# Optimization experiments

Measured on AMD Instinct MI355X. Metric: run time of the kernel, lower is better.

Reference implementation:

```python
import jax, jax.numpy as jnp
import numpy as np

K = 3          # conv kernel size
PW = 4         # parallel window (pw_height == pw_width)
OC = 128       # out_channels
IC = 128       # in_channels
RANK = 256
STRIDE = PW - K + 1  # 2


def _sdk_weight_map(kernel):
    # kernel: [O, C, K, K] numpy. Concat all (top,left) zero-pad placements into PWxPW.
    O, C, k, _ = kernel.shape
    d = PW - k
    maps = []
    for top in range(d + 1):
        for left in range(d + 1):
            pk = np.zeros((O, C, PW, PW), dtype=kernel.dtype)
            pk[:, :, top:top + k, left:left + k] = kernel
            maps.append(pk.reshape(O, -1))
    return np.concatenate(maps, axis=0)  # [(d+1)^2 * O, C*PW*PW]


def setup_inputs() -> dict:
    rng = np.random.default_rng(0)
    kernel = (rng.standard_normal((OC, IC, K, K)) * 0.05).astype(np.float32)
    W = _sdk_weight_map(kernel)  # [512, 2048]
    u, s, vh = np.linalg.svd(W, full_matrices=False)
    Q = (u[:, :RANK] * s[:RANK]).astype(np.float32)   # u_t @ diag(s_t)
    R = vh[:RANK].astype(np.float32)
    key = jax.random.key(0)
    x = jax.random.normal(key, (32, 128, 64, 64), dtype=jnp.float32)
    return {"x": x, "Q": jnp.asarray(Q), "R": jnp.asarray(R)}


def _slice_and_forward(x, Q, R):
    N, C, H, Wd = x.shape
    s = STRIDE
    pad_v = (H + 2 - PW) % s
    pad_h = (Wd + 2 - PW) % s
    ov = -(-(H + 2 - PW) // s) + 1   # ceil div + 1 (matches math.ceil(...)+1)
    oh = -(-(Wd + 2 - PW) // s) + 1
    xp = jnp.pad(x, ((0, 0), (0, 0), (1, 1 + pad_v), (1, 1 + pad_h)))
    # im2col / unfold: feature layout C slowest, then (i, j) within window -> matches F.unfold
    wins = [xp[:, :, i:i + s * (ov - 1) + 1:s, j:j + s * (oh - 1) + 1:s]
            for i in range(PW) for j in range(PW)]
    patches = jnp.stack(wins, axis=2)                      # [N, C, PW*PW, ov, oh]
    flat = patches.reshape(N, C * PW * PW, ov * oh).transpose(0, 2, 1)  # [N, L, C*PW*PW]
    # F.linear(flat, Q @ R) == (flat @ R^T) @ Q^T  (apply low-rank factors sequentially)
    lin = jnp.einsum('nlr,mr->nlm', jnp.einsum('nlf,rf->nlr', flat, R), Q)  # [N, L, s*s*OC]
    lin = lin.reshape(N, ov, oh, s, s, OC).transpose(0, 1, 3, 2, 4, 5)
    lin = lin.reshape(N, H + pad_v // 2, Wd + pad_h // 2, OC)
    lin = lin.transpose(0, 3, 1, 2)                        # NHWC -> NCHW
    return lin[:, :, :H, :Wd]


def reference(x, Q, R):
    return _slice_and_forward(x, Q, R)
```

## Files before the change

### kernel.cpp

```cpp
#include <hip/hip_runtime.h>
#include <hip/hip_bf16.h>

typedef __attribute__((ext_vector_type(8))) short short8;
typedef __attribute__((ext_vector_type(4))) float f32x4;
typedef unsigned int uint;
typedef __attribute__((ext_vector_type(4))) uint uint4v;

#define AS1 __attribute__((address_space(1)))
#define AS3 __attribute__((address_space(3)))

#define QB_OFF  (1u << 20)
#define XPH_OFF (1310720u)

__device__ __forceinline__ uint bf16r(float f) {
    uint u = __float_as_uint(f);
    u += 0x7FFFu + ((u >> 16) & 1u);
    return u >> 16;
}
__device__ __forceinline__ uint pk2(float lo, float hi) {
    return bf16r(lo) | (bf16r(hi) << 16);
}

__global__ __launch_bounds__(256) void prep_kernel(
    const float* __restrict__ x, const float* __restrict__ Q, const float* __restrict__ R,
    char* __restrict__ Rp4, char* __restrict__ Qp4, char* __restrict__ xph)
{
    const int bid = blockIdx.x, tid = threadIdx.x;
    if (bid < 2048) {
        __shared__ float xt[128 * 65];
        const int n = bid >> 6, h = bid & 63;
        {
            const int c = tid >> 1, half = tid & 1;
            const float4* src = (const float4*)(x + (((size_t)(n * 128 + c) * 64 + h) * 64 + half * 32));
            #pragma unroll
            for (int q = 0; q < 8; ++q) {
                float4 v = src[q];
                float* d = &xt[c * 65 + half * 32 + q * 4];
                d[0] = v.x; d[1] = v.y; d[2] = v.z; d[3] = v.w;
            }
        }
        __syncthreads();
        {
            const int w = tid >> 2, cq = tid & 3;
            uint pw[16];
            #pragma unroll
            for (int m = 0; m < 16; ++m)
                pw[m] = pk2(xt[(cq * 32 + 2 * m) * 65 + w], xt[(cq * 32 + 2 * m + 1) * 65 + w]);
            char* dst = xph + (size_t)n * 1115136 + (size_t)(h + 1) * 16896 + (w + 1) * 256 + cq * 64;
            #pragma unroll
            for (int i = 0; i < 4; ++i) {
                uint4v q4 = { pw[4 * i], pw[4 * i + 1], pw[4 * i + 2], pw[4 * i + 3] };
                *(uint4v*)(dst + i * 16) = q4;
            }
        }
        if (tid < 32) {
            int side = tid >> 4, e = tid & 15;
            uint4v z = {0, 0, 0, 0};
            *(uint4v*)(xph + (size_t)n * 1115136 + (size_t)(h + 1) * 16896 + side * 65 * 256 + e * 16) = z;
        }
        if (h == 0) {
            uint4v z = {0, 0, 0, 0};
            #pragma unroll
            for (int it = 0; it < 9; ++it) {
                int idx = tid + it * 256;
                if (idx < 2112) {
                    int rr = (idx >= 1056) ? 65 : 0;
                    int jj = idx - (rr ? 1056 : 0);
                    int col = jj >> 4, e = jj & 15;
                    *(uint4v*)(xph + (size_t)n * 1115136 + (size_t)rr * 16896 + col * 256 + e * 16) = z;
                }
            }
        }
    } else if (bid < 2304) {
        int g = (bid - 2048) * 256 + tid;
        int s = g >> 10, rem = g & 1023;
        int cu = rem >> 8, col = rem & 255;
        const float* src = R + (size_t)col * 2048 + (((s & 3) * 32 + cu * 8) * 16 + (s >> 2));
        uint pw[4];
        #pragma unroll
        for (int m = 0; m < 4; ++m)
            pw[m] = pk2(src[(2 * m) * 16], src[(2 * m + 1) * 16]);
        uint4v q4 = { pw[0], pw[1], pw[2], pw[3] };
        *(uint4v*)(Rp4 + (size_t)g * 16) = q4;
    } else {
        int g = (bid - 2304) * 256 + tid;
        int ks = g >> 11, p = g & 2047;
        int col = p >> 2, cu = p & 3;
        const float4* s = (const float4*)(Q + (size_t)col * 256 + ks * 32 + cu * 8);
        float4 a = s[0], b = s[1];
        uint4v q4 = { pk2(a.x, a.y), pk2(a.z, a.w), pk2(b.x, b.y), pk2(b.z, b.w) };
        *(uint4v*)(Qp4 + (size_t)ks * 32768 + p * 16) = q4;
    }
}

__global__ __launch_bounds__(256, 2) void fused_kernel(
    const char* __restrict__ xph, const char* __restrict__ Rp4,
    const char* __restrict__ Qp4, float* __restrict__ out)
{
    extern __shared__ __align__(16) char lds[];

    const int blk = blockIdx.x;
    const int b = (blk & 7) * 64 + (blk >> 3);
    const int n = b >> 4, vt = b & 15;
    const int tid = threadIdx.x;
    const int wave = tid >> 6, lane = tid & 63;
    const int lr = lane & 15, kg = lane >> 4;
    const int lr7 = lr & 7;
    const int wn = wave;

    const char* xbase = xph + (size_t)n * 1115136;
    const int u16 = tid * 16;

    const int xrh = lane >> 5, xcl = lane & 31;
    const int xc0 = (4 * vt + 2 * xrh) * 16896 + (2 * xcl) * 256 + wave * 16;

    const int a0  = kg * 1024 + lr * 16;
    const int bb0 = kg * 4096 + wn * 1024 + lr * 16;

    const int t0 = (wn * 8 + (lr >> 3)) * 1024 + (lr & 7) * 2;

    int qoff[8];
    #pragma unroll
    for (int nf = 0; nf < 8; ++nf)
        qoff[nf] = ((wn >> 1) * 256 + (nf >> 2) * 128 + (wn & 1) * 64 + (nf & 3) * 16 + lr) * 64 + kg * 16;

#define BDMA(s_) { _Pragma("unroll") for (int q = 0; q < 4; ++q)                        \
        __builtin_amdgcn_global_load_lds(                                               \
            (const AS1 void*)(Rp4 + (size_t)(s_) * 16384 + q * 4096 + u16),             \
            (AS3 void*)(lds + 12288 + ((s_) % 3) * 16384 + q * 4096 + u16), 16, 0, 0); }
#define XDMA(s_) __builtin_amdgcn_global_load_lds(                                      \
        (const AS1 void*)(xbase + xc0 + ((s_) >> 4) * 16896 + (((s_) >> 2) & 3) * 256 + ((s_) & 3) * 64), \
        (AS3 void*)(lds + ((s_) % 3) * 4096 + u16), 16, 0, 0);

#define BAR(Nstr) { __builtin_amdgcn_sched_barrier(0);                                  \
        asm volatile("s_waitcnt vmcnt(" Nstr ") lgkmcnt(0)\n\ts_barrier" ::: "memory"); \
        __builtin_amdgcn_sched_barrier(0); }
#define LBAR { __builtin_amdgcn_sched_barrier(0);                                       \
        asm volatile("s_waitcnt lgkmcnt(0)\n\ts_barrier" ::: "memory");                 \
        __builtin_amdgcn_sched_barrier(0); }

    f32x4 acc[4][4];
    #pragma unroll
    for (int i = 0; i < 4; ++i)
        #pragma unroll
        for (int j = 0; j < 4; ++j) acc[i][j] = (f32x4)0.f;

    BDMA(0) XDMA(0) BDMA(1) XDMA(1)
    BAR("5")

    #pragma unroll
    for (int s = 0; s < 64; ++s) {
        if (s <= 61) { BDMA(s + 2) XDMA(s + 2) }
        const char* xs = lds + (s % 3) * 4096;
        const char* bs = lds + 12288 + (s % 3) * 16384;
        short8 af[4], bf[4];
        #pragma unroll
        for (int mf = 0; mf < 4; ++mf)
            af[mf] = *(const short8*)(xs + a0 + mf * 256);
        #pragma unroll
        for (int nf = 0; nf < 4; ++nf)
            bf[nf] = *(const short8*)(bs + bb0 + nf * 256);
        __builtin_amdgcn_s_setprio(1);
        #pragma unroll
        for (int nf = 0; nf < 4; ++nf)
            #pragma unroll
            for (int mf = 0; mf < 4; ++mf)
                acc[mf][nf] = __builtin_amdgcn_mfma_f32_16x16x32_bf16(af[mf], bf[nf], acc[mf][nf], 0, 0, 0);
        __builtin_amdgcn_s_setprio(0);
        if (s <= 61) { BAR("5") } else { BAR("0") }
    }

    #pragma unroll
    for (int mf = 0; mf < 4; ++mf)
        #pragma unroll
        for (int nf = 0; nf < 4; ++nf)
            #pragma unroll
            for (int r = 0; r < 4; ++r) {
                *(ushort*)(lds + t0 + nf * 2048 + (mf * 16 + kg * 4 + r) * 16) =
                    (ushort)bf16r(acc[mf][nf][r]);
            }
    LBAR

    f32x4 acc2[4][8];
    #pragma unroll
    for (int i = 0; i < 4; ++i)
        #pragma unroll
        for (int j = 0; j < 8; ++j) acc2[i][j] = (f32x4)0.f;
    #pragma unroll
    for (int ks = 0; ks < 8; ++ks) {
        short8 af2[4];
        #pragma unroll
        for (int mf = 0; mf < 4; ++mf)
            af2[mf] = *(const short8*)(lds + ks * 4096 + a0 + mf * 256);
        #pragma unroll
        for (int nf = 0; nf < 8; ++nf) {
            const short8 bq = *(const short8*)(Qp4 + (size_t)ks * 32768 + qoff[nf]);
            #pragma unroll
            for (int mf = 0; mf < 4; ++mf)
                acc2[mf][nf] = __builtin_amdgcn_mfma_f32_16x16x32_bf16(af2[mf], bq, acc2[mf][nf], 0, 0, 0);
        }
    }

    const int si = wn >> 1, ochalf = wn & 1;
    #pragma unroll
    for (int p = 0; p < 2; ++p) {
        LBAR
        #pragma unroll
        for (int mfh = 0; mfh < 2; ++mfh) {
            const int mf = 2 * p + mfh;
            #pragma unroll
            for (int q = 0; q < 4; ++q) {
                const int oc = ochalf * 64 + q * 16 + lr;
                const int ub = si * 32768 + oc * 256 + (((4 * mfh + kg) ^ lr7) << 5);
                f32x4 v0 = { acc2[mf][q][0], acc2[mf][4 + q][0], acc2[mf][q][1], acc2[mf][4 + q][1] };
                f32x4 v1 = { acc2[mf][q][2], acc2[mf][4 + q][2], acc2[mf][q][3], acc2[mf][4 + q][3] };
                *(f32x4*)(lds + ub) = v0;
                *(f32x4*)(lds + ub + 16) = v1;
            }
        }
        LBAR
        #pragma unroll
        for (int it = 0; it < 16; ++it) {
            int uidx = it * 256 + tid;
            int w4 = uidx & 15, oc = (uidx >> 4) & 127, sie = uidx >> 11;
            f32x4 v = *(const f32x4*)(lds + sie * 32768 + oc * 256 + ((w4 ^ (2 * (oc & 7))) << 4));
            *(f32x4*)(out + (size_t)n * 524288 + (size_t)oc * 4096
                          + (vt * 4 + p * 2 + sie) * 64 + w4 * 4) = v;
        }
    }
}

extern "C" void kernel_launch(void* const* d_in, const int* in_sizes, int n_in,
                              void* d_out, int out_size, void* d_ws, size_t ws_size,
                              hipStream_t stream) {
    const float* x = (const float*)d_in[0];
    const float* Q = (const float*)d_in[1];
    const float* R = (const float*)d_in[2];
    float* out = (float*)d_out;

    char* ws = (char*)d_ws;
    char* Rp4 = ws;
    char* Qp4 = ws + QB_OFF;
    char* xph = ws + XPH_OFF;

    prep_kernel<<<2368, 256, 0, stream>>>(x, Q, R, Rp4, Qp4, xph);
    fused_kernel<<<512, 256, 65536, stream>>>(xph, Rp4, Qp4, out);
}
```

Before: 89.42 us.

## Load GEMM1 fragments directly from global with register double-buffering, drop LDS staging

The first low-rank GEMM no longer stages x patches and R tiles through a triple-buffered LDS pipeline with per-step barriers. Each wave now loads its MFMA fragments straight from global memory into two register sets that alternate, so loads overlap compute without barriers. The second GEMM is split into two halves to lower live accumulator registers, its results are written directly to global instead of going through an LDS transpose, LDS drops to 32KB and the occupancy hint rises to 3 blocks. The risks are redundant global/L2 traffic, since waves no longer share staged tiles, and less coalesced output stores.

```diff
diff --git a/kernel.cpp b/kernel.cpp
--- a/kernel.cpp
+++ b/kernel.cpp
@@ -93,7 +93,7 @@
     }
 }
 
-__global__ __launch_bounds__(256, 2) void fused_kernel(
+__global__ __launch_bounds__(256, 3) void fused_kernel(
     const char* __restrict__ xph, const char* __restrict__ Rp4,
     const char* __restrict__ Qp4, float* __restrict__ out)
 {
@@ -105,128 +105,100 @@
     const int tid = threadIdx.x;
     const int wave = tid >> 6, lane = tid & 63;
     const int lr = lane & 15, kg = lane >> 4;
-    const int lr7 = lr & 7;
     const int wn = wave;
 
-    const char* xbase = xph + (size_t)n * 1115136;
-    const int u16 = tid * 16;
-
-    const int xrh = lane >> 5, xcl = lane & 31;
-    const int xc0 = (4 * vt + 2 * xrh) * 16896 + (2 * xcl) * 256 + wave * 16;
-
-    const int a0  = kg * 1024 + lr * 16;
-    const int bb0 = kg * 4096 + wn * 1024 + lr * 16;
-
-    const int t0 = (wn * 8 + (lr >> 3)) * 1024 + (lr & 7) * 2;
-
+    const char* xbase = xph + (size_t)n * 1115136 + (size_t)(4 * vt) * 16896;
+    const int xv0 = lr * 512 + kg * 16;
+    const int bv0 = kg * 4096 + (wn * 64 + lr) * 16;
+
+    f32x4 acc[4][4];
+    #pragma unroll
+    for (int i = 0; i < 4; ++i)
+        #pragma unroll
+        for (int j = 0; j < 4; ++j) acc[i][j] = (f32x4)0.f;
+
+    short8 afA[4], bfA[4], afB[4], bfB[4];
+
+#define LOADA(dst_, s_) { \
+        const char* xp_ = xbase + ((s_) >> 4) * 16896 + (((s_) >> 2) & 3) * 256 + ((s_) & 3) * 64 + xv0; \
+        dst_[0] = *(const short8*)(xp_);             \
+        dst_[1] = *(const short8*)(xp_ + 8192);      \
+        dst_[2] = *(const short8*)(xp_ + 33792);     \
+        dst_[3] = *(const short8*)(xp_ + 41984); }
+#define LOADB(dst_, s_) { \
+        const char* rp_ = Rp4 + (size_t)(s_) * 16384 + bv0; \
+        _Pragma("unroll") for (int nf = 0; nf < 4; ++nf) \
+            dst_[nf] = *(const short8*)(rp_ + nf * 256); }
+#define MFMA16(af_, bf_) { \
+        __builtin_amdgcn_s_setprio(1); \
+        _Pragma("unroll") for (int nf = 0; nf < 4; ++nf) \
+            _Pragma("unroll") for (int mf = 0; mf < 4; ++mf) \
+                acc[mf][nf] = __builtin_amdgcn_mfma_f32_16x16x32_bf16(af_[mf], bf_[nf], acc[mf][nf], 0, 0, 0); \
+        __builtin_amdgcn_s_setprio(0); }
+
+    LOADA(afA, 0) LOADB(bfA, 0)
+    LOADA(afB, 1) LOADB(bfB, 1)
+
+    #pragma unroll 4
+    for (int s = 0; s < 64; s += 2) {
+        MFMA16(afA, bfA);
+        if (s < 62) { LOADA(afA, s + 2) LOADB(bfA, s + 2) }
+        MFMA16(afB, bfB);
+        if (s <= 60) { LOADA(afB, s + 3) LOADB(bfB, s + 3) }
+    }
+
+    {
+        const int t0 = (wn * 8 + (lr >> 3)) * 1024 + (lr & 7) * 2;
+        #pragma unroll
+        for (int mf = 0; mf < 4; ++mf)
+            #pragma unroll
+            for (int nf = 0; nf < 4; ++nf)
+                #pragma unroll
+                for (int r = 0; r < 4; ++r)
+                    *(ushort*)(lds + t0 + nf * 2048 + (mf * 16 + kg * 4 + r) * 16) =
+                        (ushort)bf16r(acc[mf][nf][r]);
+    }
+    __syncthreads();
+
+    const int a2base = kg * 1024 + lr * 16;
     int qoff[8];
     #pragma unroll
     for (int nf = 0; nf < 8; ++nf)
         qoff[nf] = ((wn >> 1) * 256 + (nf >> 2) * 128 + (wn & 1) * 64 + (nf & 3) * 16 + lr) * 64 + kg * 16;
-
-#define BDMA(s_) { _Pragma("unroll") for (int q = 0; q < 4; ++q)                        \
-        __builtin_amdgcn_global_load_lds(                                               \
-            (const AS1 void*)(Rp4 + (size_t)(s_) * 16384 + q * 4096 + u16),             \
-            (AS3 void*)(lds + 12288 + ((s_) % 3) * 16384 + q * 4096 + u16), 16, 0, 0); }
-#define XDMA(s_) __builtin_amdgcn_global_load_lds(                                      \
-        (const AS1 void*)(xbase + xc0 + ((s_) >> 4) * 16896 + (((s_) >> 2) & 3) * 256 + ((s_) & 3) * 64), \
-        (AS3 void*)(lds + ((s_) % 3) * 4096 + u16), 16, 0, 0);
-
-#define BAR(Nstr) { __builtin_amdgcn_sched_barrier(0);                                  \
-        asm volatile("s_waitcnt vmcnt(" Nstr ") lgkmcnt(0)\n\ts_barrier" ::: "memory"); \
-        __builtin_amdgcn_sched_barrier(0); }
-#define LBAR { __builtin_amdgcn_sched_barrier(0);                                       \
-        asm volatile("s_waitcnt lgkmcnt(0)\n\ts_barrier" ::: "memory");                 \
-        __builtin_amdgcn_sched_barrier(0); }
-
-    f32x4 acc[4][4];
+    const int si = wn >> 1, ochalf = wn & 1;
+
     #pragma unroll
-    for (int i = 0; i < 4; ++i)
-        #pragma unroll
-        for (int j = 0; j < 4; ++j) acc[i][j] = (f32x4)0.f;
-
-    BDMA(0) XDMA(0) BDMA(1) XDMA(1)
-    BAR("5")
-
-    #pragma unroll
-    for (int s = 0; s < 64; ++s) {
-        if (s <= 61) { BDMA(s + 2) XDMA(s + 2) }
-        const char* xs = lds + (s % 3) * 4096;
-        const char* bs = lds + 12288 + (s % 3) * 16384;
-        short8 af[4], bf[4];
-        #pragma unroll
-        for (int mf = 0; mf < 4; ++mf)
-            af[mf] = *(const short8*)(xs + a0 + mf * 256);
-        #pragma unroll
-        for (int nf = 0; nf < 4; ++nf)
-            bf[nf] = *(const short8*)(bs + bb0 + nf * 256);
-        __builtin_amdgcn_s_setprio(1);
-        #pragma unroll
-        for (int nf = 0; nf < 4; ++nf)
-            #pragma unroll
-            for (int mf = 0; mf < 4; ++mf)
-                acc[mf][nf] = __builtin_amdgcn_mfma_f32_16x16x32_bf16(af[mf], bf[nf], acc[mf][nf], 0, 0, 0);
-        __builtin_amdgcn_s_setprio(0);
-        if (s <= 61) { BAR("5") } else { BAR("0") }
-    }
-
-    #pragma unroll
-    for (int mf = 0; mf < 4; ++mf)
-        #pragma unroll
-        for (int nf = 0; nf < 4; ++nf)
-            #pragma unroll
-            for (int r = 0; r < 4; ++r) {
-                *(ushort*)(lds + t0 + nf * 2048 + (mf * 16 + kg * 4 + r) * 16) =
-                    (ushort)bf16r(acc[mf][nf][r]);
-            }
-    LBAR
-
-    f32x4 acc2[4][8];
-    #pragma unroll
-    for (int i = 0; i < 4; ++i)
-        #pragma unroll
-        for (int j = 0; j < 8; ++j) acc2[i][j] = (f32x4)0.f;
-    #pragma unroll
-    for (int ks = 0; ks < 8; ++ks) {
-        short8 af2[4];
-        #pragma unroll
-        for (int mf = 0; mf < 4; ++mf)
-            af2[mf] = *(const short8*)(lds + ks * 4096 + a0 + mf * 256);
-        #pragma unroll
-        for (int nf = 0; nf < 8; ++nf) {
-            const short8 bq = *(const short8*)(Qp4 + (size_t)ks * 32768 + qoff[nf]);
-            #pragma unroll
-            for (int mf = 0; mf < 4; ++mf)
-                acc2[mf][nf] = __builtin_amdgcn_mfma_f32_16x16x32_bf16(af2[mf], bq, acc2[mf][nf], 0, 0, 0);
-        }
-    }
-
-    const int si = wn >> 1, ochalf = wn & 1;
-    #pragma unroll
-    for (int p = 0; p < 2; ++p) {
-        LBAR
-        #pragma unroll
-        for (int mfh = 0; mfh < 2; ++mfh) {
-            const int mf = 2 * p + mfh;
+    for (int mh2 = 0; mh2 < 2; ++mh2) {
+        f32x4 a2[2][8];
+        #pragma unroll
+        for (int u = 0; u < 2; ++u)
+            #pragma unroll
+            for (int j = 0; j < 8; ++j) a2[u][j] = (f32x4)0.f;
+        #pragma unroll
+        for (int ks = 0; ks < 8; ++ks) {
+            short8 af2[2];
+            af2[0] = *(const short8*)(lds + ks * 4096 + a2base + (mh2 * 2) * 256);
+            af2[1] = *(const short8*)(lds + ks * 4096 + a2base + (mh2 * 2 + 1) * 256);
+            #pragma unroll
+            for (int nf = 0; nf < 8; ++nf) {
+                const short8 bq = *(const short8*)(Qp4 + (size_t)ks * 32768 + qoff[nf]);
+                a2[0][nf] = __builtin_amdgcn_mfma_f32_16x16x32_bf16(af2[0], bq, a2[0][nf], 0, 0, 0);
+                a2[1][nf] = __builtin_amdgcn_mfma_f32_16x16x32_bf16(af2[1], bq, a2[1][nf], 0, 0, 0);
+            }
+        }
+        const int r_out = vt * 4 + mh2 * 2 + si;
+        float* ob = out + (size_t)n * 524288 + (size_t)r_out * 64;
+        #pragma unroll
+        for (int u = 0; u < 2; ++u)
             #pragma unroll
             for (int q = 0; q < 4; ++q) {
                 const int oc = ochalf * 64 + q * 16 + lr;
-                const int ub = si * 32768 + oc * 256 + (((4 * mfh + kg) ^ lr7) << 5);
-                f32x4 v0 = { acc2[mf][q][0], acc2[mf][4 + q][0], acc2[mf][q][1], acc2[mf][4 + q][1] };
-                f32x4 v1 = { acc2[mf][q][2], acc2[mf][4 + q][2], acc2[mf][q][3], acc2[mf][4 + q][3] };
-                *(f32x4*)(lds + ub) = v0;
-                *(f32x4*)(lds + ub + 16) = v1;
-            }
-        }
-        LBAR
-        #pragma unroll
-        for (int it = 0; it < 16; ++it) {
-            int uidx = it * 256 + tid;
-            int w4 = uidx & 15, oc = (uidx >> 4) & 127, sie = uidx >> 11;
-            f32x4 v = *(const f32x4*)(lds + sie * 32768 + oc * 256 + ((w4 ^ (2 * (oc & 7))) << 4));
-            *(f32x4*)(out + (size_t)n * 524288 + (size_t)oc * 4096
-                          + (vt * 4 + p * 2 + sie) * 64 + w4 * 4) = v;
-        }
+                float* o2 = ob + (size_t)oc * 4096 + u * 32 + kg * 8;
+                f32x4 v0 = { a2[u][q][0], a2[u][4 + q][0], a2[u][q][1], a2[u][4 + q][1] };
+                f32x4 v1 = { a2[u][q][2], a2[u][4 + q][2], a2[u][q][3], a2[u][4 + q][3] };
+                *(f32x4*)(o2) = v0;
+                *(f32x4*)(o2 + 4) = v1;
+            }
     }
 }
 
@@ -244,5 +216,5 @@
     char* xph = ws + XPH_OFF;
 
     prep_kernel<<<2368, 256, 0, stream>>>(x, Q, R, Rp4, Qp4, xph);
-    fused_kernel<<<512, 256, 65536, stream>>>(xph, Rp4, Qp4, out);
-}
+    fused_kernel<<<512, 256, 32768, stream>>>(xph, Rp4, Qp4, out);
+}
```

Result: slower. 130.1 us (+45.5%).

## Double block tile to 512 threads with 4-stage pipeline and direct output stores

Applied to the files above, without the earlier changes.

Each workgroup now processes twice as many output rows (128-row M tile split across 2x4 waves), so every R tile loaded into LDS is reused by twice as many rows. Grid size is halved and the block size doubled. The LDS ring grows from 3 to 4 stages with prefetch distance 3, and a barrier is added after the fragment loads. The epilogue drops the LDS transpose staging and writes accumulators straight to global memory, saving barriers and LDS traffic at the cost of less coalesced stores. LDS use rises to 96KB per block, which may limit occupancy.

```diff
diff --git a/kernel.cpp b/kernel.cpp
--- a/kernel.cpp
+++ b/kernel.cpp
@@ -93,51 +93,43 @@
     }
 }
 
-__global__ __launch_bounds__(256, 2) void fused_kernel(
+__global__ __launch_bounds__(512, 2) void fused_kernel(
     const char* __restrict__ xph, const char* __restrict__ Rp4,
     const char* __restrict__ Qp4, float* __restrict__ out)
 {
     extern __shared__ __align__(16) char lds[];
 
     const int blk = blockIdx.x;
-    const int b = (blk & 7) * 64 + (blk >> 3);
-    const int n = b >> 4, vt = b & 15;
+    const int b = (blk & 7) * 32 + (blk >> 3);
+    const int n = b >> 3, vt = b & 7;
     const int tid = threadIdx.x;
     const int wave = tid >> 6, lane = tid & 63;
     const int lr = lane & 15, kg = lane >> 4;
-    const int lr7 = lr & 7;
-    const int wn = wave;
+    const int wm = wave >> 2, wn = wave & 3;
 
     const char* xbase = xph + (size_t)n * 1115136;
     const int u16 = tid * 16;
 
-    const int xrh = lane >> 5, xcl = lane & 31;
-    const int xc0 = (4 * vt + 2 * xrh) * 16896 + (2 * xcl) * 256 + wave * 16;
-
-    const int a0  = kg * 1024 + lr * 16;
-    const int bb0 = kg * 4096 + wn * 1024 + lr * 16;
-
-    const int t0 = (wn * 8 + (lr >> 3)) * 1024 + (lr & 7) * 2;
-
-    int qoff[8];
-    #pragma unroll
-    for (int nf = 0; nf < 8; ++nf)
-        qoff[nf] = ((wn >> 1) * 256 + (nf >> 2) * 128 + (wn & 1) * 64 + (nf & 3) * 16 + lr) * 64 + kg * 16;
-
-#define BDMA(s_) { _Pragma("unroll") for (int q = 0; q < 4; ++q)                        \
-        __builtin_amdgcn_global_load_lds(                                               \
-            (const AS1 void*)(Rp4 + (size_t)(s_) * 16384 + q * 4096 + u16),             \
-            (AS3 void*)(lds + 12288 + ((s_) % 3) * 16384 + q * 4096 + u16), 16, 0, 0); }
-#define XDMA(s_) __builtin_amdgcn_global_load_lds(                                      \
-        (const AS1 void*)(xbase + xc0 + ((s_) >> 4) * 16896 + (((s_) >> 2) & 3) * 256 + ((s_) & 3) * 64), \
-        (AS3 void*)(lds + ((s_) % 3) * 4096 + u16), 16, 0, 0);
-
-#define BAR(Nstr) { __builtin_amdgcn_sched_barrier(0);                                  \
+    const int xc = (8 * vt + 2 * ((tid >> 5) & 3)) * 16896 + (tid & 31) * 512 + (tid >> 7) * 16;
+
+    const int a0 = kg * 2048 + (wm * 64 + lr) * 16;
+    const int b0 = kg * 4096 + (wn * 64 + lr) * 16;
+
+#define STAGE(t_) { \
+        __builtin_amdgcn_global_load_lds( \
+            (const AS1 void*)(xbase + xc + ((t_) >> 4) * 16896 + (((t_) >> 2) & 3) * 256 + ((t_) & 3) * 64), \
+            (AS3 void*)(lds + ((t_) & 3) * 8192 + u16), 16, 0, 0); \
+        _Pragma("unroll") for (int q = 0; q < 2; ++q) \
+            __builtin_amdgcn_global_load_lds( \
+                (const AS1 void*)(Rp4 + (size_t)(t_) * 16384 + q * 8192 + u16), \
+                (AS3 void*)(lds + 32768 + ((t_) & 3) * 16384 + q * 8192 + u16), 16, 0, 0); }
+
+#define BAR1 { __builtin_amdgcn_sched_barrier(0); \
+        asm volatile("s_barrier\n\ts_waitcnt lgkmcnt(0)" ::: "memory"); \
+        __builtin_amdgcn_sched_barrier(0); }
+#define BAR(Nstr) { __builtin_amdgcn_sched_barrier(0); \
         asm volatile("s_waitcnt vmcnt(" Nstr ") lgkmcnt(0)\n\ts_barrier" ::: "memory"); \
         __builtin_amdgcn_sched_barrier(0); }
-#define LBAR { __builtin_amdgcn_sched_barrier(0);                                       \
-        asm volatile("s_waitcnt lgkmcnt(0)\n\ts_barrier" ::: "memory");                 \
-        __builtin_amdgcn_sched_barrier(0); }
 
     f32x4 acc[4][4];
     #pragma unroll
@@ -145,21 +137,22 @@
         #pragma unroll
         for (int j = 0; j < 4; ++j) acc[i][j] = (f32x4)0.f;
 
-    BDMA(0) XDMA(0) BDMA(1) XDMA(1)
-    BAR("5")
-
-    #pragma unroll
-    for (int s = 0; s < 64; ++s) {
-        if (s <= 61) { BDMA(s + 2) XDMA(s + 2) }
-        const char* xs = lds + (s % 3) * 4096;
-        const char* bs = lds + 12288 + (s % 3) * 16384;
+    STAGE(0) STAGE(1) STAGE(2)
+    BAR("6")
+
+    #pragma unroll
+    for (int t = 0; t < 64; ++t) {
+        if (t <= 60) STAGE(t + 3)
+        const char* xs = lds + (t & 3) * 8192;
+        const char* bs = lds + 32768 + (t & 3) * 16384;
         short8 af[4], bf[4];
         #pragma unroll
         for (int mf = 0; mf < 4; ++mf)
             af[mf] = *(const short8*)(xs + a0 + mf * 256);
         #pragma unroll
         for (int nf = 0; nf < 4; ++nf)
-            bf[nf] = *(const short8*)(bs + bb0 + nf * 256);
+            bf[nf] = *(const short8*)(bs + b0 + nf * 256);
+        BAR1
         __builtin_amdgcn_s_setprio(1);
         #pragma unroll
         for (int nf = 0; nf < 4; ++nf)
@@ -167,19 +160,32 @@
             for (int mf = 0; mf < 4; ++mf)
                 acc[mf][nf] = __builtin_amdgcn_mfma_f32_16x16x32_bf16(af[mf], bf[nf], acc[mf][nf], 0, 0, 0);
         __builtin_amdgcn_s_setprio(0);
-        if (s <= 61) { BAR("5") } else { BAR("0") }
-    }
-
-    #pragma unroll
-    for (int mf = 0; mf < 4; ++mf)
-        #pragma unroll
-        for (int nf = 0; nf < 4; ++nf)
-            #pragma unroll
-            for (int r = 0; r < 4; ++r) {
-                *(ushort*)(lds + t0 + nf * 2048 + (mf * 16 + kg * 4 + r) * 16) =
-                    (ushort)bf16r(acc[mf][nf][r]);
-            }
-    LBAR
+        if (t <= 60)      { BAR("6") }
+        else if (t == 61) { BAR("3") }
+        else              { BAR("0") }
+    }
+
+    {
+        const int t0 = (wn * 8 + (lr >> 3)) * 2048 + wm * 1024 + (lr & 7) * 2;
+        #pragma unroll
+        for (int mf = 0; mf < 4; ++mf)
+            #pragma unroll
+            for (int nf = 0; nf < 4; ++nf)
+                #pragma unroll
+                for (int r = 0; r < 4; ++r)
+                    *(ushort*)(lds + t0 + nf * 4096 + (mf * 16 + kg * 4 + r) * 16) =
+                        (ushort)bf16r(acc[mf][nf][r]);
+    }
+    __builtin_amdgcn_sched_barrier(0);
+    asm volatile("s_waitcnt lgkmcnt(0)\n\ts_barrier" ::: "memory");
+    __builtin_amdgcn_sched_barrier(0);
+
+    const int a2 = kg * 2048 + wm * 1024 + lr * 16;
+    int qoff[8];
+    #pragma unroll
+    for (int nf = 0; nf < 8; ++nf)
+        qoff[nf] = ((wn >> 1) * 256 + (nf >> 2) * 128 + (wn & 1) * 64 + (nf & 3) * 16 + lr) * 64 + kg * 16;
+    const int si = wn >> 1, ochalf = wn & 1;
 
     f32x4 acc2[4][8];
     #pragma unroll
@@ -191,7 +197,7 @@
         short8 af2[4];
         #pragma unroll
         for (int mf = 0; mf < 4; ++mf)
-            af2[mf] = *(const short8*)(lds + ks * 4096 + a0 + mf * 256);
+            af2[mf] = *(const short8*)(lds + ks * 8192 + a2 + mf * 256);
         #pragma unroll
         for (int nf = 0; nf < 8; ++nf) {
             const short8 bq = *(const short8*)(Qp4 + (size_t)ks * 32768 + qoff[nf]);
@@ -201,31 +207,18 @@
         }
     }
 
-    const int si = wn >> 1, ochalf = wn & 1;
-    #pragma unroll
-    for (int p = 0; p < 2; ++p) {
-        LBAR
-        #pragma unroll
-        for (int mfh = 0; mfh < 2; ++mfh) {
-            const int mf = 2 * p + mfh;
-            #pragma unroll
-            for (int q = 0; q < 4; ++q) {
-                const int oc = ochalf * 64 + q * 16 + lr;
-                const int ub = si * 32768 + oc * 256 + (((4 * mfh + kg) ^ lr7) << 5);
-                f32x4 v0 = { acc2[mf][q][0], acc2[mf][4 + q][0], acc2[mf][q][1], acc2[mf][4 + q][1] };
-                f32x4 v1 = { acc2[mf][q][2], acc2[mf][4 + q][2], acc2[mf][q][3], acc2[mf][4 + q][3] };
-                *(f32x4*)(lds + ub) = v0;
-                *(f32x4*)(lds + ub + 16) = v1;
-            }
-        }
-        LBAR
-        #pragma unroll
-        for (int it = 0; it < 16; ++it) {
-            int uidx = it * 256 + tid;
-            int w4 = uidx & 15, oc = (uidx >> 4) & 127, sie = uidx >> 11;
-            f32x4 v = *(const f32x4*)(lds + sie * 32768 + oc * 256 + ((w4 ^ (2 * (oc & 7))) << 4));
-            *(f32x4*)(out + (size_t)n * 524288 + (size_t)oc * 4096
-                          + (vt * 4 + p * 2 + sie) * 64 + w4 * 4) = v;
+    #pragma unroll
+    for (int mf = 0; mf < 4; ++mf) {
+        const int h = 8 * vt + 4 * wm + 2 * (mf >> 1) + si;
+        float* ob = out + (size_t)n * 524288 + (size_t)h * 64 + (mf & 1) * 32 + kg * 8;
+        #pragma unroll
+        for (int q = 0; q < 4; ++q) {
+            const int oc = ochalf * 64 + q * 16 + lr;
+            float* o2 = ob + (size_t)oc * 4096;
+            f32x4 v0 = { acc2[mf][q][0], acc2[mf][4 + q][0], acc2[mf][q][1], acc2[mf][4 + q][1] };
+            f32x4 v1 = { acc2[mf][q][2], acc2[mf][4 + q][2], acc2[mf][q][3], acc2[mf][4 + q][3] };
+            *(f32x4*)(o2) = v0;
+            *(f32x4*)(o2 + 4) = v1;
         }
     }
 }
@@ -244,5 +237,5 @@
     char* xph = ws + XPH_OFF;
 
     prep_kernel<<<2368, 256, 0, stream>>>(x, Q, R, Rp4, Qp4, xph);
-    fused_kernel<<<512, 256, 65536, stream>>>(xph, Rp4, Qp4, out);
-}
+    fused_kernel<<<256, 512, 98304, stream>>>(xph, Rp4, Qp4, out);
+}
```

New measurement: 92.46 us. +3.4%, slower.
